# Optimization experiments

Hardware: AMD Instinct MI355X
Metric: run time of the kernel (lower is better)

## Reference

```python
import jax, jax.numpy as jnp
import numpy as np
from functools import partial

B, N, NCLS = 16, 25200, 80
M_TGT = 50
MAX_DET = 300
CONF_THRES = 0.8
NMS_THRES = 0.4


def cxcywh_to_xyxy(boxes):
    # cxcywh -> xywh -> xyxy (as in tensor_to_dict: cxcywh_to_xywh then xywh_to_xyxy)
    cx, cy, w, h = boxes[..., 0], boxes[..., 1], boxes[..., 2], boxes[..., 3]
    x1 = cx - 0.5 * w
    y1 = cy - 0.5 * h
    return jnp.stack([x1, y1, x1 + w, y1 + h], axis=-1)


def pairwise_iou(b):
    # b: [K,4] xyxy
    x1 = jnp.maximum(b[:, None, 0], b[None, :, 0])
    y1 = jnp.maximum(b[:, None, 1], b[None, :, 1])
    x2 = jnp.minimum(b[:, None, 2], b[None, :, 2])
    y2 = jnp.minimum(b[:, None, 3], b[None, :, 3])
    inter = jnp.clip(x2 - x1, 0.0) * jnp.clip(y2 - y1, 0.0)
    area = jnp.clip(b[:, 2] - b[:, 0], 0.0) * jnp.clip(b[:, 3] - b[:, 1], 0.0)
    return inter / (area[:, None] + area[None, :] - inter + 1e-9)


def nms_one(boxes_xyxy, labels, valid):
    # boxes sorted by score descending; class-aware greedy NMS, fixed K iterations
    K = boxes_xyxy.shape[0]
    iou = pairwise_iou(boxes_xyxy)
    same = labels[:, None] == labels[None, :]
    supp = (iou > NMS_THRES) & same
    idx = jnp.arange(K)

    def body(i, keep):
        kill = supp[i] & (idx > i) & keep[i]
        return keep & ~kill

    return jax.lax.fori_loop(0, K, body, valid)


def post_process(preds):
    # preds: [B, N, 5+C] (cx,cy,w,h,obj,cls...)
    obj = preds[..., 4]
    cls_prob = preds[..., 5:]
    cls_conf = jnp.max(cls_prob, axis=-1)
    cls_id = jnp.argmax(cls_prob, axis=-1)
    score = obj * cls_conf                      # [B,N]
    score = jnp.where(score > CONF_THRES, score, 0.0)
    top_s, top_i = jax.lax.top_k(score, MAX_DET)            # [B,K]
    boxes = jnp.take_along_axis(preds[..., :4], top_i[..., None], axis=1)  # cxcywh [B,K,4]
    labels = jnp.take_along_axis(cls_id, top_i, axis=1)     # [B,K]
    valid = top_s > 0.0
    boxes_xyxy = cxcywh_to_xyxy(boxes)
    keep = jax.vmap(nms_one)(boxes_xyxy, labels, valid)     # [B,K]
    scores = jnp.where(keep, top_s, 0.0)
    boxes_xyxy = jnp.where(keep[..., None], boxes_xyxy, 0.0)
    labels = jnp.where(keep, labels, -1)
    return boxes_xyxy, scores, labels, keep


def process_targets(tt, lengths):
    # tt: [B, M, 6] = cxcywh, score, label ; lengths: [B]
    valid = jnp.arange(tt.shape[1])[None, :] < lengths[:, None]  # [B,M]
    boxes = cxcywh_to_xyxy(tt[..., :4])
    scores = tt[..., 4]
    labels = tt[..., 5].astype(jnp.int32)
    boxes = jnp.where(valid[..., None], boxes, 0.0)
    scores = jnp.where(valid, scores, 0.0)
    labels = jnp.where(valid, labels, -1)
    return boxes, scores, labels, valid


def setup_inputs() -> dict:
    key = jax.random.key(0)
    k1, k2, k3, k4 = jax.random.split(key, 4)
    preds = jax.random.uniform(k1, (B, N, 5 + NCLS), dtype=jnp.float32)
    tgt_boxes = jax.random.uniform(k2, (B, M_TGT, 4), dtype=jnp.float32) * 640.0
    tgt_scores = jnp.ones((B, M_TGT, 1), dtype=jnp.float32)
    tgt_labels = jax.random.randint(k3, (B, M_TGT, 1), 0, NCLS).astype(jnp.float32)
    target_target = jnp.concatenate([tgt_boxes, tgt_scores, tgt_labels], axis=-1)
    target_lengths = jax.random.randint(k4, (B,), 1, M_TGT + 1).astype(jnp.int32)
    return {"preds": preds, "target_target": target_target, "target_lengths": target_lengths}


def reference(preds, target_target, target_lengths):
    pb, ps, pl, pv = post_process(preds)
    tb, ts, tl, tv = process_targets(target_target, target_lengths)
    # @torch.no_grad in original forward
    out = (pb, ps, pl, pv, tb, ts, tl, tv)
    return jax.tree_util.tree_map(jax.lax.stop_gradient, out)
```

## Files before the change

kernel.cpp:

```cpp
#include <hip/hip_runtime.h>
#include <cstdint>

#define BB 16
#define NN 25200
#define NCLS 80
#define NF (5 + NCLS)
#define MAXDET 300
#define MTGT 50
#define CONF 0.8f
#define NMSTH 0.4f
#define WORDS 10
#define NBINS 2048
#define SBUF 2048
#define APB 64
#define SCORE_BLOCKS ((BB * NN) / APB)
#define TGT_BLOCKS ((BB * MTGT + 255) / 256)

#define WS_SCORE 0
#define WS_DS   ((size_t)BB * NN * 4)
#define WS_DI   (WS_DS + (size_t)BB * MAXDET * 4)
#define WS_GBOX (WS_DI + (size_t)BB * MAXDET * 4)
#define WS_GLAB (WS_GBOX + (size_t)BB * MAXDET * 16)

#define O_PB 0
#define O_PS (BB * MAXDET * 4)
#define O_PL (O_PS + BB * MAXDET)
#define O_PV (O_PL + BB * MAXDET)
#define O_TB (O_PV + BB * MAXDET)
#define O_TS (O_TB + BB * MTGT * 4)
#define O_TL (O_TS + BB * MTGT)
#define O_TV (O_TL + BB * MTGT)

__global__ __launch_bounds__(256) void k_score(const float* __restrict__ preds,
                                               float* __restrict__ scores,
                                               const float* __restrict__ tt,
                                               const int* __restrict__ len,
                                               float* __restrict__ out) {
    __shared__ float st[APB * NF];
    int tid = threadIdx.x;

    if (blockIdx.x >= SCORE_BLOCKS) {
        int t = (blockIdx.x - SCORE_BLOCKS) * 256 + tid;
        if (t < BB * MTGT) {
            int b = t / MTGT, m = t - b * MTGT;
            const float* row = tt + (size_t)t * 6;
            bool valid = m < len[b];
            float cx = row[0], cy = row[1], w = row[2], h = row[3];
            float x1 = cx - 0.5f * w, y1 = cy - 0.5f * h;
            float* tb = out + O_TB + (size_t)t * 4;
            tb[0] = valid ? x1 : 0.f;
            tb[1] = valid ? y1 : 0.f;
            tb[2] = valid ? (x1 + w) : 0.f;
            tb[3] = valid ? (y1 + h) : 0.f;
            out[O_TS + t] = valid ? row[4] : 0.f;
            out[O_TL + t] = valid ? (float)(int)row[5] : -1.f;
            out[O_TV + t] = valid ? 1.f : 0.f;
        }
        return;
    }

    int base = blockIdx.x * APB;
    const float4* src = (const float4*)(preds + (size_t)base * NF);
    float4* dst = (float4*)st;
    #pragma unroll
    for (int i = 0; i < 6; ++i) {
        int idx = i * 256 + tid;
        if (idx < APB * NF / 4) dst[idx] = src[idx];
    }
    __syncthreads();

    int a = tid >> 2, q = tid & 3;
    const float* row = st + a * NF;
    const float* cls = row + 5 + q * 20;
    float m = cls[0];
    #pragma unroll
    for (int f = 1; f < 20; ++f) m = fmaxf(m, cls[f]);
    m = fmaxf(m, __shfl_xor(m, 1));
    m = fmaxf(m, __shfl_xor(m, 2));
    if (q == 0) scores[base + a] = row[4] * m;
}

__global__ __launch_bounds__(1024) void k_select(const float* __restrict__ scores,
                                                 float* __restrict__ dscore,
                                                 unsigned* __restrict__ didx) {
    __shared__ int hist[NBINS];
    __shared__ unsigned long long sk[SBUF];
    __shared__ int lcnt;
    __shared__ int scut;
    int b = blockIdx.x;
    int tid = threadIdx.x;
    int lane = tid & 63;

    if (tid == 0) lcnt = 0;
    for (int i = tid; i < NBINS; i += 1024) hist[i] = 0;
    for (int i = tid; i < SBUF; i += 1024) sk[i] = 0ull;
    __syncthreads();

    for (int i = tid; i < NN; i += 1024) {
        float s = scores[b * NN + i];
        if (s > CONF) {
            unsigned u = __float_as_uint(s);
            int bin = (int)((u - 0x3F400000u) >> 12);
            bin = bin < 0 ? 0 : (bin > NBINS - 1 ? NBINS - 1 : bin);
            atomicAdd(&hist[bin], 1);
        }
    }
    __syncthreads();

    if (tid < 64) {
        int sb = 0;
        #pragma unroll
        for (int k = 0; k < 32; ++k) sb += hist[tid * 32 + k];
        int cum = sb;
        #pragma unroll
        for (int d = 1; d < 64; d <<= 1) {
            int o = __shfl_down(cum, d);
            if (lane + d < 64) cum += o;
        }
        unsigned long long m = __ballot(cum >= MAXDET);
        int cutbin = 0;
        if (m) {
            int cutS = 63 - __clzll(m);
            int tail = (cutS < 63) ? __shfl(cum, cutS + 1) : 0;
            int hh = (lane < 32) ? hist[cutS * 32 + lane] : 0;
            int c2 = hh;
            #pragma unroll
            for (int d = 1; d < 32; d <<= 1) {
                int o = __shfl_down(c2, d);
                if (lane + d < 32) c2 += o;
            }
            c2 += tail;
            unsigned long long m2 = __ballot(lane < 32 && c2 >= MAXDET);
            int cutL = 63 - __clzll(m2);
            cutbin = cutS * 32 + cutL;
        }
        if (lane == 0) scut = cutbin;
    }
    __syncthreads();
    int cutbin = scut;

    for (int i = tid; i < ((NN + 1023) & ~1023); i += 1024) {
        float s = 0.f; bool pass = false;
        if (i < NN) {
            s = scores[b * NN + i];
            if (s > CONF) {
                unsigned u = __float_as_uint(s);
                int bin = (int)((u - 0x3F400000u) >> 12);
                bin = bin < 0 ? 0 : (bin > NBINS - 1 ? NBINS - 1 : bin);
                pass = bin >= cutbin;
            }
        }
        unsigned long long mask = __ballot(pass);
        int wcnt = __popcll(mask);
        int bs = 0;
        if (lane == 0 && wcnt) bs = atomicAdd(&lcnt, wcnt);
        bs = __shfl(bs, 0);
        if (pass) {
            int pos = bs + __popcll(mask & ((1ull << lane) - 1ull));
            if (pos < SBUF)
                sk[pos] = ((unsigned long long)__float_as_uint(s) << 32) |
                          (unsigned long long)(0xFFFFFFFFu - (unsigned)i);
        }
    }
    __syncthreads();

    int M = lcnt; if (M > SBUF) M = SBUF;
    unsigned P = 512;
    while ((int)P < M) P <<= 1;

    for (unsigned k = 2; k <= P; k <<= 1) {
        for (unsigned j = k >> 1; j > 0; j >>= 1) {
            __syncthreads();
            for (unsigned i = tid; i < P; i += 1024) {
                unsigned ixj = i ^ j;
                if (ixj > i) {
                    unsigned long long a = sk[i], d = sk[ixj];
                    bool desc = ((i & k) == 0);
                    if (desc ? (a < d) : (a > d)) { sk[i] = d; sk[ixj] = a; }
                }
            }
        }
    }
    __syncthreads();
    for (int q = tid; q < MAXDET; q += 1024) {
        unsigned long long key = sk[q];
        unsigned sbits = (unsigned)(key >> 32);
        dscore[b * MAXDET + q] = __uint_as_float(sbits);
        didx[b * MAXDET + q]   = sbits ? (0xFFFFFFFFu - (unsigned)(key & 0xFFFFFFFFu)) : 0u;
    }
}

__global__ __launch_bounds__(512) void k_gather(const float* __restrict__ preds,
                                                const float* __restrict__ dscore,
                                                const unsigned* __restrict__ didx,
                                                float* __restrict__ gbox,
                                                int* __restrict__ glabel) {
    int g    = blockIdx.x * 8 + (threadIdx.x >> 6);
    int lane = threadIdx.x & 63;
    float sc = dscore[g];
    if (sc > 0.f) {
        int b = g / MAXDET;
        int idx = (int)didx[g];
        const float* row = preds + ((size_t)b * NN + (size_t)idx) * NF;
        float v = row[5 + lane]; int ci = lane;
        if (lane < 16) { float v2 = row[69 + lane]; if (v2 > v) { v = v2; ci = lane + 64; } }
        #pragma unroll
        for (int m = 32; m >= 1; m >>= 1) {
            float ov = __shfl_xor(v, m);
            int   oi = __shfl_xor(ci, m);
            if (ov > v || (ov == v && oi < ci)) { v = ov; ci = oi; }
        }
        if (lane == 0) {
            float cx = row[0], cy = row[1], w = row[2], h = row[3];
            float x1 = cx - 0.5f * w, y1 = cy - 0.5f * h;
            float4 bx = { x1, y1, x1 + w, y1 + h };
            ((float4*)gbox)[g] = bx;
            glabel[g] = ci;
        }
    } else if (lane == 0) {
        float4 zz = { 0.f, 0.f, 0.f, 0.f };
        ((float4*)gbox)[g] = zz;
        glabel[g] = -1;
    }
}

__global__ __launch_bounds__(1024) void k_nms2(const float* __restrict__ gbox,
                                               const int* __restrict__ glabel,
                                               const float* __restrict__ dscore,
                                               float* __restrict__ out) {
    __shared__ float4   sbox[MAXDET];
    __shared__ int      slabel[MAXDET];
    __shared__ float    sscore[MAXDET];
    __shared__ unsigned supp[MAXDET * WORDS];
    int b = blockIdx.x;
    int tid = threadIdx.x;

    if (tid < MAXDET) {
        int g = b * MAXDET + tid;
        sbox[tid]   = ((const float4*)gbox)[g];
        slabel[tid] = glabel[g];
        sscore[tid] = dscore[g];
    }
    __syncthreads();

    for (int T = tid; T < MAXDET * WORDS; T += 1024) {
        int i  = T / WORDS;
        int jw = T - i * WORDS;
        unsigned word = 0;
        int jbase = jw * 32;
        if (jbase + 31 > i) {
            float4 bi = sbox[i];
            int   li = slabel[i];
            float si = sscore[i];
            float ai = __fmul_rn(fmaxf(__fsub_rn(bi.z, bi.x), 0.f),
                                 fmaxf(__fsub_rn(bi.w, bi.y), 0.f));
            for (int tt = 0; tt < 32; ++tt) {
                int t = (tt + jw) & 31;
                int j = jbase + t;
                if (j > i && j < MAXDET) {
                    if (slabel[j] == li && si > 0.f && sscore[j] > 0.f) {
                        float4 bj = sbox[j];
                        float xx1 = fmaxf(bi.x, bj.x);
                        float yy1 = fmaxf(bi.y, bj.y);
                        float xx2 = fminf(bi.z, bj.z);
                        float yy2 = fminf(bi.w, bj.w);
                        float iw = fmaxf(__fsub_rn(xx2, xx1), 0.f);
                        float ih = fmaxf(__fsub_rn(yy2, yy1), 0.f);
                        float inter = __fmul_rn(iw, ih);
                        float aj = __fmul_rn(fmaxf(__fsub_rn(bj.z, bj.x), 0.f),
                                             fmaxf(__fsub_rn(bj.w, bj.y), 0.f));
                        float den = __fadd_rn(__fsub_rn(__fadd_rn(ai, aj), inter), 1e-9f);
                        float iou = inter / den;
                        if (iou > NMSTH) word |= 1u << t;
                    }
                }
            }
        }
        supp[T] = word;
    }
    __syncthreads();

    if (tid < 64) {
        int lane = tid;
        unsigned keep = 0, nzm = 0;
        #pragma unroll
        for (int s = 0; s < 5; ++s) {
            int k = s * 64 + lane;
            bool kb = (k < MAXDET) && (sscore[k] > 0.f);
            unsigned long long m = __ballot(kb);
            if (lane == 2 * s)     keep = (unsigned)m;
            if (lane == 2 * s + 1) keep = (unsigned)(m >> 32);
            unsigned nz = 0;
            if (k < MAXDET) {
                #pragma unroll
                for (int w = 0; w < WORDS; ++w) nz |= supp[k * WORDS + w];
            }
            unsigned long long mn = __ballot(nz != 0u);
            if (lane == 2 * s)     nzm = (unsigned)mn;
            if (lane == 2 * s + 1) nzm = (unsigned)(mn >> 32);
        }

        for (int i = 0; i < MAXDET; ++i) {
            int idx = i >> 5;
            unsigned kw = __shfl(keep, idx);
            unsigned nw = __shfl(nzm, idx);
            if (((kw & nw) >> (i & 31)) & 1u) {
                if (lane < WORDS) keep &= ~supp[i * WORDS + lane];
            }
        }

        #pragma unroll
        for (int s = 0; s < 5; ++s) {
            int k = s * 64 + lane;
            if (k < MAXDET) {
                unsigned kw = __shfl(keep, k >> 5);
                bool kp = (kw >> (k & 31)) & 1u;
                int g = b * MAXDET + k;
                float4 bx = sbox[k];
                float4 zz = { 0.f, 0.f, 0.f, 0.f };
                ((float4*)(out + O_PB))[g] = kp ? bx : zz;
                out[O_PS + g] = kp ? sscore[k] : 0.f;
                out[O_PL + g] = kp ? (float)slabel[k] : -1.f;
                out[O_PV + g] = kp ? 1.f : 0.f;
            }
        }
    }
}

extern "C" void kernel_launch(void* const* d_in, const int* in_sizes, int n_in,
                              void* d_out, int out_size, void* d_ws, size_t ws_size,
                              hipStream_t stream) {
    const float* preds = (const float*)d_in[0];
    const float* tt    = (const float*)d_in[1];
    const int*   len   = (const int*)d_in[2];
    float* out = (float*)d_out;

    char* ws = (char*)d_ws;
    float*    scores = (float*)(ws + WS_SCORE);
    float*    dscore = (float*)(ws + WS_DS);
    unsigned* didx   = (unsigned*)(ws + WS_DI);
    float*    gbox   = (float*)(ws + WS_GBOX);
    int*      glabel = (int*)(ws + WS_GLAB);

    k_score <<<SCORE_BLOCKS + TGT_BLOCKS, 256, 0, stream>>>(preds, scores, tt, len, out);
    k_select<<<BB, 1024, 0, stream>>>(scores, dscore, didx);
    k_gather<<<(BB * MAXDET) / 8, 512, 0, stream>>>(preds, dscore, didx, gbox, glabel);
    k_nms2  <<<BB, 1024, 0, stream>>>(gbox, glabel, dscore, out);
}
```

Measured before the change: 96.32 us.

## Make score kernel persistent with register-prefetched double-buffered LDS chunks

Replaces the one-block-per-64-anchor grid with a persistent grid of 768 blocks that stride over chunks. Each block prefetches the next chunk into registers while reducing the current one from a double-buffered LDS tile, and target processing is folded into the first blocks. The goal is to overlap global loads with compute and cut block launch overhead in this bandwidth-bound pass, at the cost of more LDS per block and possibly lower occupancy. The chunk count (6300) does not divide evenly by 768, so the last pass is unbalanced across blocks.

```diff
diff --git a/kernel.cpp b/kernel.cpp
--- a/kernel.cpp
+++ b/kernel.cpp
@@ -13,8 +13,10 @@
 #define NBINS 2048
 #define SBUF 2048
 #define APB 64
-#define SCORE_BLOCKS ((BB * NN) / APB)
+#define NCHUNK ((BB * NN) / APB)
+#define PBLK 768
 #define TGT_BLOCKS ((BB * MTGT + 255) / 256)
+#define CHUNK_V4 (APB * NF / 4)
 
 #define WS_SCORE 0
 #define WS_DS   ((size_t)BB * NN * 4)
@@ -36,11 +38,12 @@
                                                const float* __restrict__ tt,
                                                const int* __restrict__ len,
                                                float* __restrict__ out) {
-    __shared__ float st[APB * NF];
+    __shared__ float st[2][APB * NF];
     int tid = threadIdx.x;
-
-    if (blockIdx.x >= SCORE_BLOCKS) {
-        int t = (blockIdx.x - SCORE_BLOCKS) * 256 + tid;
+    int bid = blockIdx.x;
+
+    if (bid < TGT_BLOCKS) {
+        int t = bid * 256 + tid;
         if (t < BB * MTGT) {
             int b = t / MTGT, m = t - b * MTGT;
             const float* row = tt + (size_t)t * 6;
@@ -56,28 +59,60 @@
             out[O_TL + t] = valid ? (float)(int)row[5] : -1.f;
             out[O_TV + t] = valid ? 1.f : 0.f;
         }
-        return;
-    }
-
-    int base = blockIdx.x * APB;
-    const float4* src = (const float4*)(preds + (size_t)base * NF);
-    float4* dst = (float4*)st;
-    #pragma unroll
-    for (int i = 0; i < 6; ++i) {
-        int idx = i * 256 + tid;
-        if (idx < APB * NF / 4) dst[idx] = src[idx];
-    }
-    __syncthreads();
-
-    int a = tid >> 2, q = tid & 3;
-    const float* row = st + a * NF;
-    const float* cls = row + 5 + q * 20;
-    float m = cls[0];
-    #pragma unroll
-    for (int f = 1; f < 20; ++f) m = fmaxf(m, cls[f]);
-    m = fmaxf(m, __shfl_xor(m, 1));
-    m = fmaxf(m, __shfl_xor(m, 2));
-    if (q == 0) scores[base + a] = row[4] * m;
+    }
+
+    int c = bid;
+    float4 r[6];
+
+    {
+        const float4* src = (const float4*)(preds + (size_t)c * (APB * NF));
+        #pragma unroll
+        for (int i = 0; i < 6; ++i) {
+            int idx = i * 256 + tid;
+            if (idx < CHUNK_V4) r[i] = src[idx];
+        }
+        #pragma unroll
+        for (int i = 0; i < 6; ++i) {
+            int idx = i * 256 + tid;
+            if (idx < CHUNK_V4) ((float4*)st[0])[idx] = r[i];
+        }
+    }
+    __syncthreads();
+
+    int cur = 0;
+    while (true) {
+        int nc = c + PBLK;
+        bool have_next = nc < NCHUNK;
+        if (have_next) {
+            const float4* src = (const float4*)(preds + (size_t)nc * (APB * NF));
+            #pragma unroll
+            for (int i = 0; i < 6; ++i) {
+                int idx = i * 256 + tid;
+                if (idx < CHUNK_V4) r[i] = src[idx];
+            }
+        }
+
+        {
+            int a = tid >> 2, q = tid & 3;
+            const float* row = st[cur] + a * NF;
+            const float* cls = row + 5 + q * 20;
+            float m = cls[0];
+            #pragma unroll
+            for (int f = 1; f < 20; ++f) m = fmaxf(m, cls[f]);
+            m = fmaxf(m, __shfl_xor(m, 1));
+            m = fmaxf(m, __shfl_xor(m, 2));
+            if (q == 0) scores[c * APB + a] = row[4] * m;
+        }
+
+        if (!have_next) break;
+        #pragma unroll
+        for (int i = 0; i < 6; ++i) {
+            int idx = i * 256 + tid;
+            if (idx < CHUNK_V4) ((float4*)st[cur ^ 1])[idx] = r[i];
+        }
+        __syncthreads();
+        cur ^= 1; c = nc;
+    }
 }
 
 __global__ __launch_bounds__(1024) void k_select(const float* __restrict__ scores,
@@ -342,7 +377,7 @@
     float*    gbox   = (float*)(ws + WS_GBOX);
     int*      glabel = (int*)(ws + WS_GLAB);
 
-    k_score <<<SCORE_BLOCKS + TGT_BLOCKS, 256, 0, stream>>>(preds, scores, tt, len, out);
+    k_score <<<PBLK, 256, 0, stream>>>(preds, scores, tt, len, out);
     k_select<<<BB, 1024, 0, stream>>>(scores, dscore, didx);
     k_gather<<<(BB * MAXDET) / 8, 512, 0, stream>>>(preds, dscore, didx, gbox, glabel);
     k_nms2  <<<BB, 1024, 0, stream>>>(gbox, glabel, dscore, out);
```

After: 124.7 us. 1.3x slower.

## Fuse select, gather and NMS into one kernel; async LDS loads in scoring

Applied to the files above, without the earlier changes.

Merges the top-k selection, box/label gather and NMS kernels into a single per-image kernel that keeps candidates in shared memory. This removes two launches and the workspace round-trips between them. The scoring kernel now uses 128-thread blocks and direct global-to-LDS loads, with two threads per anchor doing a four-way unrolled class max. The fused kernel needs more shared memory per block and runs the gather on only 16 blocks, so that step has less parallelism.

```diff
diff --git a/kernel.cpp b/kernel.cpp
--- a/kernel.cpp
+++ b/kernel.cpp
@@ -13,14 +13,11 @@
 #define NBINS 2048
 #define SBUF 2048
 #define APB 64
+#define CHUNK_V4 (APB * NF / 4)
 #define SCORE_BLOCKS ((BB * NN) / APB)
-#define TGT_BLOCKS ((BB * MTGT + 255) / 256)
+#define NTGT_BLOCKS ((BB * MTGT + 127) / 128)
 
 #define WS_SCORE 0
-#define WS_DS   ((size_t)BB * NN * 4)
-#define WS_DI   (WS_DS + (size_t)BB * MAXDET * 4)
-#define WS_GBOX (WS_DI + (size_t)BB * MAXDET * 4)
-#define WS_GLAB (WS_GBOX + (size_t)BB * MAXDET * 16)
 
 #define O_PB 0
 #define O_PS (BB * MAXDET * 4)
@@ -31,16 +28,17 @@
 #define O_TL (O_TS + BB * MTGT)
 #define O_TV (O_TL + BB * MTGT)
 
-__global__ __launch_bounds__(256) void k_score(const float* __restrict__ preds,
+__global__ __launch_bounds__(128) void k_score(const float* __restrict__ preds,
                                                float* __restrict__ scores,
                                                const float* __restrict__ tt,
                                                const int* __restrict__ len,
                                                float* __restrict__ out) {
     __shared__ float st[APB * NF];
     int tid = threadIdx.x;
-
-    if (blockIdx.x >= SCORE_BLOCKS) {
-        int t = (blockIdx.x - SCORE_BLOCKS) * 256 + tid;
+    int bid = blockIdx.x;
+
+    if (bid >= SCORE_BLOCKS) {
+        int t = (bid - SCORE_BLOCKS) * 128 + tid;
         if (t < BB * MTGT) {
             int b = t / MTGT, m = t - b * MTGT;
             const float* row = tt + (size_t)t * 6;
@@ -59,32 +57,42 @@
         return;
     }
 
-    int base = blockIdx.x * APB;
-    const float4* src = (const float4*)(preds + (size_t)base * NF);
-    float4* dst = (float4*)st;
+    int w = tid >> 6;
+    const float4* src = (const float4*)(preds + (size_t)bid * (APB * NF));
     #pragma unroll
-    for (int i = 0; i < 6; ++i) {
-        int idx = i * 256 + tid;
-        if (idx < APB * NF / 4) dst[idx] = src[idx];
-    }
-    __syncthreads();
-
-    int a = tid >> 2, q = tid & 3;
-    const float* row = st + a * NF;
-    const float* cls = row + 5 + q * 20;
-    float m = cls[0];
+    for (int i = 0; i < 11; ++i) {
+        int idx = i * 128 + tid;
+        if (idx < CHUNK_V4) {
+            __builtin_amdgcn_global_load_lds(
+                (const __attribute__((address_space(1))) void*)(src + idx),
+                (__attribute__((address_space(3))) void*)(st + (i * 128 + w * 64) * 4),
+                16, 0, 0);
+        }
+    }
+    __syncthreads();
+
+    int a = tid >> 1, h = tid & 1;
+    const float* cls = st + a * NF + 5 + h * 40;
+    float m0 = cls[0], m1 = cls[1], m2 = cls[2], m3 = cls[3];
     #pragma unroll
-    for (int f = 1; f < 20; ++f) m = fmaxf(m, cls[f]);
+    for (int f = 4; f < 40; f += 4) {
+        m0 = fmaxf(m0, cls[f]);     m1 = fmaxf(m1, cls[f + 1]);
+        m2 = fmaxf(m2, cls[f + 2]); m3 = fmaxf(m3, cls[f + 3]);
+    }
+    float m = fmaxf(fmaxf(m0, m1), fmaxf(m2, m3));
     m = fmaxf(m, __shfl_xor(m, 1));
-    m = fmaxf(m, __shfl_xor(m, 2));
-    if (q == 0) scores[base + a] = row[4] * m;
+    if (h == 0) scores[bid * APB + a] = st[a * NF + 4] * m;
 }
 
-__global__ __launch_bounds__(1024) void k_select(const float* __restrict__ scores,
-                                                 float* __restrict__ dscore,
-                                                 unsigned* __restrict__ didx) {
+__global__ __launch_bounds__(1024) void k_post(const float* __restrict__ scores,
+                                               const float* __restrict__ preds,
+                                               float* __restrict__ out) {
     __shared__ int hist[NBINS];
     __shared__ unsigned long long sk[SBUF];
+    __shared__ float4   sbox[MAXDET];
+    __shared__ int      slabel[MAXDET];
+    __shared__ float    sscore[MAXDET];
+    __shared__ unsigned supp[MAXDET * WORDS];
     __shared__ int lcnt;
     __shared__ int scut;
     int b = blockIdx.x;
@@ -182,64 +190,36 @@
         }
     }
     __syncthreads();
-    for (int q = tid; q < MAXDET; q += 1024) {
-        unsigned long long key = sk[q];
-        unsigned sbits = (unsigned)(key >> 32);
-        dscore[b * MAXDET + q] = __uint_as_float(sbits);
-        didx[b * MAXDET + q]   = sbits ? (0xFFFFFFFFu - (unsigned)(key & 0xFFFFFFFFu)) : 0u;
-    }
-}
-
-__global__ __launch_bounds__(512) void k_gather(const float* __restrict__ preds,
-                                                const float* __restrict__ dscore,
-                                                const unsigned* __restrict__ didx,
-                                                float* __restrict__ gbox,
-                                                int* __restrict__ glabel) {
-    int g    = blockIdx.x * 8 + (threadIdx.x >> 6);
-    int lane = threadIdx.x & 63;
-    float sc = dscore[g];
-    if (sc > 0.f) {
-        int b = g / MAXDET;
-        int idx = (int)didx[g];
-        const float* row = preds + ((size_t)b * NN + (size_t)idx) * NF;
-        float v = row[5 + lane]; int ci = lane;
-        if (lane < 16) { float v2 = row[69 + lane]; if (v2 > v) { v = v2; ci = lane + 64; } }
-        #pragma unroll
-        for (int m = 32; m >= 1; m >>= 1) {
-            float ov = __shfl_xor(v, m);
-            int   oi = __shfl_xor(ci, m);
-            if (ov > v || (ov == v && oi < ci)) { v = ov; ci = oi; }
-        }
-        if (lane == 0) {
-            float cx = row[0], cy = row[1], w = row[2], h = row[3];
-            float x1 = cx - 0.5f * w, y1 = cy - 0.5f * h;
-            float4 bx = { x1, y1, x1 + w, y1 + h };
-            ((float4*)gbox)[g] = bx;
-            glabel[g] = ci;
-        }
-    } else if (lane == 0) {
-        float4 zz = { 0.f, 0.f, 0.f, 0.f };
-        ((float4*)gbox)[g] = zz;
-        glabel[g] = -1;
-    }
-}
-
-__global__ __launch_bounds__(1024) void k_nms2(const float* __restrict__ gbox,
-                                               const int* __restrict__ glabel,
-                                               const float* __restrict__ dscore,
-                                               float* __restrict__ out) {
-    __shared__ float4   sbox[MAXDET];
-    __shared__ int      slabel[MAXDET];
-    __shared__ float    sscore[MAXDET];
-    __shared__ unsigned supp[MAXDET * WORDS];
-    int b = blockIdx.x;
-    int tid = threadIdx.x;
-
-    if (tid < MAXDET) {
-        int g = b * MAXDET + tid;
-        sbox[tid]   = ((const float4*)gbox)[g];
-        slabel[tid] = glabel[g];
-        sscore[tid] = dscore[g];
+
+    {
+        int wv = tid >> 6;
+        for (int k = wv; k < MAXDET; k += 16) {
+            unsigned long long key = sk[k];
+            unsigned sbits = (unsigned)(key >> 32);
+            if (sbits) {
+                int idx = (int)(0xFFFFFFFFu - (unsigned)(key & 0xFFFFFFFFu));
+                const float* row = preds + ((size_t)b * NN + (size_t)idx) * NF;
+                float v = row[5 + lane]; int ci = lane;
+                if (lane < 16) { float v2 = row[69 + lane]; if (v2 > v) { v = v2; ci = lane + 64; } }
+                #pragma unroll
+                for (int m = 32; m >= 1; m >>= 1) {
+                    float ov = __shfl_xor(v, m);
+                    int   oi = __shfl_xor(ci, m);
+                    if (ov > v || (ov == v && oi < ci)) { v = ov; ci = oi; }
+                }
+                if (lane == 0) {
+                    float cx = row[0], cy = row[1], w = row[2], h = row[3];
+                    float x1 = cx - 0.5f * w, y1 = cy - 0.5f * h;
+                    float4 bx = { x1, y1, x1 + w, y1 + h };
+                    sbox[k] = bx;
+                    slabel[k] = ci;
+                    sscore[k] = __uint_as_float(sbits);
+                }
+            } else if (lane == 0) {
+                float4 zz = { 0.f, 0.f, 0.f, 0.f };
+                sbox[k] = zz; slabel[k] = -1; sscore[k] = 0.f;
+            }
+        }
     }
     __syncthreads();
 
@@ -254,8 +234,8 @@
             float si = sscore[i];
             float ai = __fmul_rn(fmaxf(__fsub_rn(bi.z, bi.x), 0.f),
                                  fmaxf(__fsub_rn(bi.w, bi.y), 0.f));
-            for (int tt = 0; tt < 32; ++tt) {
-                int t = (tt + jw) & 31;
+            for (int uu = 0; uu < 32; ++uu) {
+                int t = (uu + jw) & 31;
                 int j = jbase + t;
                 if (j > i && j < MAXDET) {
                     if (slabel[j] == li && si > 0.f && sscore[j] > 0.f) {
@@ -281,7 +261,6 @@
     __syncthreads();
 
     if (tid < 64) {
-        int lane = tid;
         unsigned keep = 0, nzm = 0;
         #pragma unroll
         for (int s = 0; s < 5; ++s) {
@@ -335,15 +314,8 @@
     const int*   len   = (const int*)d_in[2];
     float* out = (float*)d_out;
 
-    char* ws = (char*)d_ws;
-    float*    scores = (float*)(ws + WS_SCORE);
-    float*    dscore = (float*)(ws + WS_DS);
-    unsigned* didx   = (unsigned*)(ws + WS_DI);
-    float*    gbox   = (float*)(ws + WS_GBOX);
-    int*      glabel = (int*)(ws + WS_GLAB);
-
-    k_score <<<SCORE_BLOCKS + TGT_BLOCKS, 256, 0, stream>>>(preds, scores, tt, len, out);
-    k_select<<<BB, 1024, 0, stream>>>(scores, dscore, didx);
-    k_gather<<<(BB * MAXDET) / 8, 512, 0, stream>>>(preds, dscore, didx, gbox, glabel);
-    k_nms2  <<<BB, 1024, 0, stream>>>(gbox, glabel, dscore, out);
+    float* scores = (float*)((char*)d_ws + WS_SCORE);
+
+    k_score<<<SCORE_BLOCKS + NTGT_BLOCKS, 128, 0, stream>>>(preds, scores, tt, len, out);
+    k_post <<<BB, 1024, 0, stream>>>(scores, preds, out);
 }
```

After: 111.2 us. 15.5% more time.

## Use direct global-to-LDS loads in scoring and selection, pad histogram

Applied to the files above, without the earlier changes.

The score kernel now uses 128-thread blocks, loads its prediction chunk straight into LDS with global_load_lds, and computes the class max with two threads per anchor using four independent accumulators. The select kernel stages a full batch row of scores in LDS once, so both passes read LDS instead of global memory twice. It also pads the histogram stride to 33 to reduce LDS bank conflicts. In exchange the select kernel uses about 100KB of LDS per block, and the correctness of the async LDS load layout has to be relied on.

```diff
diff --git a/kernel.cpp b/kernel.cpp
--- a/kernel.cpp
+++ b/kernel.cpp
@@ -13,8 +13,10 @@
 #define NBINS 2048
 #define SBUF 2048
 #define APB 64
+#define CHUNK_V4 (APB * NF / 4)
 #define SCORE_BLOCKS ((BB * NN) / APB)
-#define TGT_BLOCKS ((BB * MTGT + 255) / 256)
+#define NTGT_BLOCKS ((BB * MTGT + 127) / 128)
+#define HSTRIDE 33
 
 #define WS_SCORE 0
 #define WS_DS   ((size_t)BB * NN * 4)
@@ -31,16 +33,17 @@
 #define O_TL (O_TS + BB * MTGT)
 #define O_TV (O_TL + BB * MTGT)
 
-__global__ __launch_bounds__(256) void k_score(const float* __restrict__ preds,
+__global__ __launch_bounds__(128) void k_score(const float* __restrict__ preds,
                                                float* __restrict__ scores,
                                                const float* __restrict__ tt,
                                                const int* __restrict__ len,
                                                float* __restrict__ out) {
     __shared__ float st[APB * NF];
     int tid = threadIdx.x;
-
-    if (blockIdx.x >= SCORE_BLOCKS) {
-        int t = (blockIdx.x - SCORE_BLOCKS) * 256 + tid;
+    int bid = blockIdx.x;
+
+    if (bid >= SCORE_BLOCKS) {
+        int t = (bid - SCORE_BLOCKS) * 128 + tid;
         if (t < BB * MTGT) {
             int b = t / MTGT, m = t - b * MTGT;
             const float* row = tt + (size_t)t * 6;
@@ -59,50 +62,70 @@
         return;
     }
 
-    int base = blockIdx.x * APB;
-    const float4* src = (const float4*)(preds + (size_t)base * NF);
-    float4* dst = (float4*)st;
+    int w = tid >> 6;
+    const float4* src = (const float4*)(preds + (size_t)bid * (APB * NF));
     #pragma unroll
-    for (int i = 0; i < 6; ++i) {
-        int idx = i * 256 + tid;
-        if (idx < APB * NF / 4) dst[idx] = src[idx];
-    }
-    __syncthreads();
-
-    int a = tid >> 2, q = tid & 3;
-    const float* row = st + a * NF;
-    const float* cls = row + 5 + q * 20;
-    float m = cls[0];
+    for (int i = 0; i < 11; ++i) {
+        int idx = i * 128 + tid;
+        if (idx < CHUNK_V4) {
+            __builtin_amdgcn_global_load_lds(
+                (const __attribute__((address_space(1))) void*)(src + idx),
+                (__attribute__((address_space(3))) void*)(st + (i * 128 + w * 64) * 4),
+                16, 0, 0);
+        }
+    }
+    __syncthreads();
+
+    int a = tid >> 1, h = tid & 1;
+    const float* cls = st + a * NF + 5 + h * 40;
+    float m0 = cls[0], m1 = cls[1], m2 = cls[2], m3 = cls[3];
     #pragma unroll
-    for (int f = 1; f < 20; ++f) m = fmaxf(m, cls[f]);
+    for (int f = 4; f < 40; f += 4) {
+        m0 = fmaxf(m0, cls[f]);     m1 = fmaxf(m1, cls[f + 1]);
+        m2 = fmaxf(m2, cls[f + 2]); m3 = fmaxf(m3, cls[f + 3]);
+    }
+    float m = fmaxf(fmaxf(m0, m1), fmaxf(m2, m3));
     m = fmaxf(m, __shfl_xor(m, 1));
-    m = fmaxf(m, __shfl_xor(m, 2));
-    if (q == 0) scores[base + a] = row[4] * m;
+    if (h == 0) scores[bid * APB + a] = st[a * NF + 4] * m;
 }
 
 __global__ __launch_bounds__(1024) void k_select(const float* __restrict__ scores,
                                                  float* __restrict__ dscore,
                                                  unsigned* __restrict__ didx) {
-    __shared__ int hist[NBINS];
+    __shared__ float sc[NN];
+    __shared__ int hist[64 * HSTRIDE];
     __shared__ unsigned long long sk[SBUF];
     __shared__ int lcnt;
     __shared__ int scut;
     int b = blockIdx.x;
     int tid = threadIdx.x;
     int lane = tid & 63;
+    int w = tid >> 6;
 
     if (tid == 0) lcnt = 0;
-    for (int i = tid; i < NBINS; i += 1024) hist[i] = 0;
+    for (int i = tid; i < 64 * HSTRIDE; i += 1024) hist[i] = 0;
     for (int i = tid; i < SBUF; i += 1024) sk[i] = 0ull;
+
+    const float4* src = (const float4*)(scores + (size_t)b * NN);
+    #pragma unroll
+    for (int i = 0; i < 7; ++i) {
+        int idx = i * 1024 + tid;
+        if (idx < NN / 4) {
+            __builtin_amdgcn_global_load_lds(
+                (const __attribute__((address_space(1))) void*)(src + idx),
+                (__attribute__((address_space(3))) void*)(sc + (i * 1024 + w * 64) * 4),
+                16, 0, 0);
+        }
+    }
     __syncthreads();
 
     for (int i = tid; i < NN; i += 1024) {
-        float s = scores[b * NN + i];
+        float s = sc[i];
         if (s > CONF) {
             unsigned u = __float_as_uint(s);
             int bin = (int)((u - 0x3F400000u) >> 12);
             bin = bin < 0 ? 0 : (bin > NBINS - 1 ? NBINS - 1 : bin);
-            atomicAdd(&hist[bin], 1);
+            atomicAdd(&hist[(bin >> 5) * HSTRIDE + (bin & 31)], 1);
         }
     }
     __syncthreads();
@@ -110,7 +133,7 @@
     if (tid < 64) {
         int sb = 0;
         #pragma unroll
-        for (int k = 0; k < 32; ++k) sb += hist[tid * 32 + k];
+        for (int k = 0; k < 32; ++k) sb += hist[lane * HSTRIDE + k];
         int cum = sb;
         #pragma unroll
         for (int d = 1; d < 64; d <<= 1) {
@@ -122,7 +145,7 @@
         if (m) {
             int cutS = 63 - __clzll(m);
             int tail = (cutS < 63) ? __shfl(cum, cutS + 1) : 0;
-            int hh = (lane < 32) ? hist[cutS * 32 + lane] : 0;
+            int hh = (lane < 32) ? hist[cutS * HSTRIDE + lane] : 0;
             int c2 = hh;
             #pragma unroll
             for (int d = 1; d < 32; d <<= 1) {
@@ -142,7 +165,7 @@
     for (int i = tid; i < ((NN + 1023) & ~1023); i += 1024) {
         float s = 0.f; bool pass = false;
         if (i < NN) {
-            s = scores[b * NN + i];
+            s = sc[i];
             if (s > CONF) {
                 unsigned u = __float_as_uint(s);
                 int bin = (int)((u - 0x3F400000u) >> 12);
@@ -254,8 +277,8 @@
             float si = sscore[i];
             float ai = __fmul_rn(fmaxf(__fsub_rn(bi.z, bi.x), 0.f),
                                  fmaxf(__fsub_rn(bi.w, bi.y), 0.f));
-            for (int tt = 0; tt < 32; ++tt) {
-                int t = (tt + jw) & 31;
+            for (int uu = 0; uu < 32; ++uu) {
+                int t = (uu + jw) & 31;
                 int j = jbase + t;
                 if (j > i && j < MAXDET) {
                     if (slabel[j] == li && si > 0.f && sscore[j] > 0.f) {
@@ -342,7 +365,7 @@
     float*    gbox   = (float*)(ws + WS_GBOX);
     int*      glabel = (int*)(ws + WS_GLAB);
 
-    k_score <<<SCORE_BLOCKS + TGT_BLOCKS, 256, 0, stream>>>(preds, scores, tt, len, out);
+    k_score <<<SCORE_BLOCKS + NTGT_BLOCKS, 128, 0, stream>>>(preds, scores, tt, len, out);
     k_select<<<BB, 1024, 0, stream>>>(scores, dscore, didx);
     k_gather<<<(BB * MAXDET) / 8, 512, 0, stream>>>(preds, dscore, didx, gbox, glabel);
     k_nms2  <<<BB, 1024, 0, stream>>>(gbox, glabel, dscore, out);
```

Result: faster. 90.19 us (-6.4%).
